# Optimization experiments

Measured on AMD Instinct MI355X. Metric: run time of the kernel, lower is better.

Reference implementation:

```python
import jax, jax.numpy as jnp
import numpy as np

N = 50000   # nodes
E = 200000  # edges (avg degree ~4, pose-graph-like sparsity)
F_IN = 512
NEG_SLOPE = 0.01  # F.leaky_relu default


def _softmax_aggr(src_feat, dst, num_nodes):
    # torch_geometric SoftmaxAggregation(t=1): per-destination, per-feature
    # alpha = softmax(x_j), out = sum_j alpha * x_j
    m = jax.ops.segment_max(src_feat, dst, num_segments=num_nodes)  # [N,F]
    m = jnp.where(jnp.isfinite(m), m, 0.0)  # empty segments -> -inf guard
    e = jnp.exp(src_feat - m[dst])                                   # [E,F]
    denom = jax.ops.segment_sum(e, dst, num_segments=num_nodes)      # [N,F]
    num = jax.ops.segment_sum(e * src_feat, dst, num_segments=num_nodes)
    return num / jnp.maximum(denom, 1e-16)  # 0 for isolated nodes


def setup_inputs() -> dict:
    key = jax.random.key(0)
    ks = jax.random.split(key, 9)
    inp = {
        "x": jax.random.normal(ks[0], (N, F_IN), dtype=jnp.float32),
        "W1_rel": jax.random.normal(ks[1], (513, 256), dtype=jnp.float32) * 0.04,
        "b1_rel": jnp.zeros((256,), dtype=jnp.float32),
        "W1_root": jax.random.normal(ks[2], (513, 256), dtype=jnp.float32) * 0.04,
        "W2_rel": jax.random.normal(ks[3], (257, 64), dtype=jnp.float32) * 0.06,
        "b2_rel": jnp.zeros((64,), dtype=jnp.float32),
        "W2_root": jax.random.normal(ks[4], (257, 64), dtype=jnp.float32) * 0.06,
        "Wp": jax.random.normal(ks[5], (65, 3), dtype=jnp.float32) * 0.1,
        "bp": jnp.zeros((3,), dtype=jnp.float32),
        "Wr": jax.random.normal(ks[6], (65, 4), dtype=jnp.float32) * 0.1,
        "br": jnp.zeros((4,), dtype=jnp.float32),
        "edge_index": jax.random.randint(ks[7], (2, E), 0, N, dtype=jnp.int64),
    }
    return inp


def reference(x, W1_rel, b1_rel, W1_root, W2_rel, b2_rel, W2_root,
              Wp, bp, Wr, br, edge_index):
    src, dst = edge_index[0], edge_index[1]
    node_index = jnp.arange(x.shape[0], dtype=x.dtype)[:, None]  # [N,1]

    # dropout is identity in eval mode
    h = jnp.concatenate([x, node_index], axis=1)  # [N,513]

    # GraphConv(513,256, aggr='softmax'): lin_rel(softmax_aggr(x_j)) + lin_root(x)
    agg1 = _softmax_aggr(h[src], dst, x.shape[0])               # [N,513]
    h = agg1 @ W1_rel + b1_rel + h @ W1_root                     # [N,256]
    h = jnp.where(h >= 0, h, NEG_SLOPE * h)

    h = jnp.concatenate([h, node_index], axis=1)  # [N,257]

    # GraphConv(257,64) default aggr='add'
    agg2 = jax.ops.segment_sum(h[src], dst, num_segments=x.shape[0])  # [N,257]
    h = agg2 @ W2_rel + b2_rel + h @ W2_root                           # [N,64]
    h = jnp.where(h >= 0, h, NEG_SLOPE * h)

    h = jnp.concatenate([h, node_index], axis=1)  # [N,65]

    position = h @ Wp + bp                         # [N,3]
    rotation = h @ Wr + br                         # [N,4]
    norm = jnp.linalg.norm(rotation, axis=1, keepdims=True)
    rotation = rotation / jnp.maximum(norm, 1e-12)  # F.normalize

    return jnp.concatenate([position, rotation], axis=1)  # [N,7]
```

## Files before the change

kernel.cpp:

```cpp
#include <hip/hip_runtime.h>

#define NNODES 50000
#define NEDGES 200000
#define NSCANB ((NNODES + 255) / 256)

typedef short  bf16x8 __attribute__((ext_vector_type(8)));
typedef float  f32x4  __attribute__((ext_vector_type(4)));
typedef unsigned int u32x4 __attribute__((ext_vector_type(4)));

__device__ __forceinline__ unsigned short f2bf(float f) {
    union { float f; unsigned int u; } c; c.f = f;
    unsigned int r = c.u + 0x7fffu + ((c.u >> 16) & 1u);
    return (unsigned short)(r >> 16);
}
__device__ __forceinline__ float bf2f(unsigned short h) {
    union { unsigned int u; float f; } c; c.u = ((unsigned int)h) << 16;
    return c.f;
}

#define PREP_Z NNODES
#define PREP_B1 (256 * 1024)
#define PREP_B2 (64 * 512)
#define PREP_XC (NNODES * 64)
#define PREP_TOT (PREP_Z + PREP_B1 + PREP_B2 + PREP_XC)
__global__ __launch_bounds__(256) void k_prep(const float* __restrict__ x,
                                              const float* __restrict__ W1_rel,
                                              const float* __restrict__ W1_root,
                                              const float* __restrict__ W2_rel,
                                              const float* __restrict__ W2_root,
                                              int* __restrict__ deg,
                                              unsigned short* __restrict__ Bt1,
                                              unsigned short* __restrict__ Bt2,
                                              unsigned short* __restrict__ xb) {
    int i = blockIdx.x * 256 + threadIdx.x;
    if (i < PREP_Z) { deg[i] = 0; return; }
    i -= PREP_Z;
    if (i < PREP_B1) {
        int n = i >> 10, k = i & 1023;
        float v = (k < 512) ? W1_rel[k * 256 + n] : W1_root[(k - 512) * 256 + n];
        Bt1[i] = f2bf(v);
        return;
    }
    i -= PREP_B1;
    if (i < PREP_B2) {
        int n = i >> 9, k = i & 511;
        float v = (k < 256) ? W2_rel[k * 64 + n] : W2_root[(k - 256) * 64 + n];
        Bt2[i] = f2bf(v);
        return;
    }
    i -= PREP_B2;
    if (i < PREP_XC) {
        int n = i >> 6, c8 = (i & 63) * 8;
        const float* xp = x + (size_t)n * 512 + c8;
        float4 a = *(const float4*)xp;
        float4 b = *(const float4*)(xp + 4);
        unsigned short o[8];
        o[0] = f2bf(a.x); o[1] = f2bf(a.y); o[2] = f2bf(a.z); o[3] = f2bf(a.w);
        o[4] = f2bf(b.x); o[5] = f2bf(b.y); o[6] = f2bf(b.z); o[7] = f2bf(b.w);
        *(u32x4*)(xb + (size_t)n * 512 + c8) = *(const u32x4*)o;
    }
}

__global__ void k_count(const int* __restrict__ ei, int* __restrict__ deg) {
    int e = blockIdx.x * 256 + threadIdx.x;
    if (e < NEDGES) atomicAdd(&deg[ei[NEDGES + e]], 1);
}

__global__ __launch_bounds__(256) void k_scanA(const int* __restrict__ deg,
                                               int* __restrict__ rs,
                                               int* __restrict__ partials) {
    __shared__ int sm[256];
    int t = threadIdx.x, i = blockIdx.x * 256 + t;
    int v = (i < NNODES) ? deg[i] : 0;
    sm[t] = v;
    __syncthreads();
#pragma unroll
    for (int off = 1; off < 256; off <<= 1) {
        int u = (t >= off) ? sm[t - off] : 0;
        __syncthreads();
        sm[t] += u;
        __syncthreads();
    }
    if (i < NNODES) rs[i] = sm[t] - v;
    if (t == 255) partials[blockIdx.x] = sm[255];
}

__global__ __launch_bounds__(256) void k_scanB(int* __restrict__ partials) {
    __shared__ int sm[256];
    int t = threadIdx.x;
    int v = (t < NSCANB) ? partials[t] : 0;
    sm[t] = v;
    __syncthreads();
#pragma unroll
    for (int off = 1; off < 256; off <<= 1) {
        int u = (t >= off) ? sm[t - off] : 0;
        __syncthreads();
        sm[t] += u;
        __syncthreads();
    }
    if (t < NSCANB) partials[t] = sm[t] - v;
}

__global__ __launch_bounds__(256) void k_scanC(int* __restrict__ rs,
                                               const int* __restrict__ partials,
                                               int* __restrict__ cursor) {
    int t = threadIdx.x, b = blockIdx.x, i = b * 256 + t;
    if (i < NNODES) {
        int v = rs[i] + partials[b];
        rs[i] = v;
        cursor[i] = v;
    }
    if (i == 0) rs[NNODES] = NEDGES;
}

__global__ void k_scatter(const int* __restrict__ ei, int* __restrict__ cursor,
                          int* __restrict__ srcs) {
    int e = blockIdx.x * 256 + threadIdx.x;
    if (e < NEDGES) {
        int d = ei[NEDGES + e];
        int p = atomicAdd(&cursor[d], 1);
        srcs[p] = ei[e];
    }
}

__global__ __launch_bounds__(256) void k_agg1(const unsigned short* __restrict__ xb,
                                              const int* __restrict__ rs,
                                              const int* __restrict__ srcs,
                                              unsigned short* __restrict__ AggBuf,
                                              float* __restrict__ aggidx,
                                              float* __restrict__ sidx) {
    int n = blockIdx.x;
    int t = threadIdx.x;
    int e0 = rs[n], e1 = rs[n + 1];
    float d0 = 0.f, q0 = 0.f, d1 = 0.f, q1 = 0.f;
    float mI = -INFINITY, dI = 0.f, qI = 0.f, sI = 0.f;
    for (int e = e0; e < e1; ++e) {
        int s = srcs[e];
        unsigned int v = *(const unsigned int*)(xb + (size_t)s * 512 + t * 2);
        float v0 = bf2f((unsigned short)(v & 0xffffu));
        float v1 = bf2f((unsigned short)(v >> 16));
        float e0v = __expf(v0);
        float e1v = __expf(v1);
        d0 += e0v; q0 += e0v * v0;
        d1 += e1v; q1 += e1v * v1;
        if (t == 0) {
            float vi = (float)s;
            sI += vi;
            float nm = fmaxf(mI, vi);
            float sc = __expf(mI - nm), ee = __expf(vi - nm);
            dI = dI * sc + ee;
            qI = qI * sc + ee * vi;
            mI = nm;
        }
    }
    float a0 = q0 / fmaxf(d0, 1e-16f);
    float a1 = q1 / fmaxf(d1, 1e-16f);
    unsigned int o = (unsigned int)f2bf(a0) | ((unsigned int)f2bf(a1) << 16);
    *(unsigned int*)(AggBuf + (size_t)n * 512 + t * 2) = o;
    if (t == 0) {
        aggidx[n] = qI / fmaxf(dI, 1e-16f);
        sidx[n] = sI;
    }
}

__global__ __launch_bounds__(256) void k_agg2(const int* __restrict__ rs,
                                              const int* __restrict__ srcs,
                                              const unsigned short* __restrict__ H1,
                                              unsigned short* __restrict__ Seg) {
    int half = threadIdx.x >> 7;
    int t = threadIdx.x & 127;
    int n = blockIdx.x * 2 + half;
    int e0 = rs[n], e1 = rs[n + 1];
    float a0 = 0.f, a1 = 0.f;
    for (int e = e0; e < e1; ++e) {
        int s = srcs[e];
        unsigned int v = *(const unsigned int*)(H1 + (size_t)s * 256 + t * 2);
        a0 += bf2f((unsigned short)(v & 0xffffu));
        a1 += bf2f((unsigned short)(v >> 16));
    }
    unsigned int o = (unsigned int)f2bf(a0) | ((unsigned int)f2bf(a1) << 16);
    *(unsigned int*)(Seg + (size_t)n * 256 + t * 2) = o;
}

__global__ __launch_bounds__(256, 5) void k_gemm1(const unsigned short* __restrict__ A1,
                                                  const unsigned short* __restrict__ A2,
                                                  const unsigned short* __restrict__ Bt,
                                                  const float* __restrict__ s1,
                                                  const float* __restrict__ r1,
                                                  const float* __restrict__ r2,
                                                  const float* __restrict__ bias,
                                                  unsigned short* __restrict__ outp) {
    constexpr int BM = 64, BN = 128, BK = 64;
    __shared__ __align__(16) unsigned short As[BM * BK];
    __shared__ __align__(16) unsigned short Bs[BN * BK];

    const int tid = threadIdx.x;
    const int w = tid >> 6;
    const int lane = tid & 63;
    const int lm = lane & 15;
    const int quad = lane >> 4;
    const int wr = w >> 1;
    const int wc = w & 1;
    const int rowbase = blockIdx.y * BM;
    const int colbase = blockIdx.x * BN;
    const int wrow = wr * 32;
    const int wcol = wc * 64;

    const int rsub = lane >> 3;
    const int csw = (lane & 7) ^ rsub;

    f32x4 acc[2][4];
#pragma unroll
    for (int mi = 0; mi < 2; ++mi)
#pragma unroll
        for (int ni = 0; ni < 4; ++ni) acc[mi][ni] = (f32x4){0.f, 0.f, 0.f, 0.f};

    for (int kt = 0; kt < 1024; kt += BK) {
        const unsigned short* Ab = (kt < 512) ? A1 : A2;
        int kof = (kt < 512) ? kt : kt - 512;
#pragma unroll
        for (int l = 0; l < 2; ++l) {
            int r = w * 16 + l * 8;
            int gr = rowbase + r + rsub;
            if (gr >= NNODES) gr = NNODES - 1;
            const unsigned short* gp = Ab + (size_t)gr * 512 + kof + csw * 8;
            __builtin_amdgcn_global_load_lds(
                (const __attribute__((address_space(1))) void*)gp,
                (__attribute__((address_space(3))) void*)(As + r * BK), 16, 0, 0);
        }
#pragma unroll
        for (int l = 0; l < 4; ++l) {
            int r = w * 32 + l * 8;
            const unsigned short* gp = Bt + (size_t)(colbase + r + rsub) * 1024 + kt + csw * 8;
            __builtin_amdgcn_global_load_lds(
                (const __attribute__((address_space(1))) void*)gp,
                (__attribute__((address_space(3))) void*)(Bs + r * BK), 16, 0, 0);
        }
        __syncthreads();
#pragma unroll
        for (int kk = 0; kk < BK; kk += 32) {
            const int kidx = (kk >> 3) + quad;
            const int phys = kidx ^ (lm & 7);
            bf16x8 af[2], bfr[4];
#pragma unroll
            for (int mi = 0; mi < 2; ++mi)
                af[mi] = __builtin_bit_cast(bf16x8,
                    *(const u32x4*)(As + (wrow + mi * 16 + lm) * BK + phys * 8));
#pragma unroll
            for (int ni = 0; ni < 4; ++ni)
                bfr[ni] = __builtin_bit_cast(bf16x8,
                    *(const u32x4*)(Bs + (wcol + ni * 16 + lm) * BK + phys * 8));
#pragma unroll
            for (int mi = 0; mi < 2; ++mi)
#pragma unroll
                for (int ni = 0; ni < 4; ++ni)
                    acc[mi][ni] = __builtin_amdgcn_mfma_f32_16x16x32_bf16(
                        af[mi], bfr[ni], acc[mi][ni], 0, 0, 0);
        }
        __syncthreads();
    }

#pragma unroll
    for (int ni = 0; ni < 4; ++ni) {
        int gc = colbase + wcol + ni * 16 + lm;
        float r1v = r1[gc], r2v = r2[gc], bv = bias[gc];
#pragma unroll
        for (int mi = 0; mi < 2; ++mi) {
#pragma unroll
            for (int r = 0; r < 4; ++r) {
                int grow = rowbase + wrow + mi * 16 + quad * 4 + r;
                if (grow < NNODES) {
                    float v = acc[mi][ni][r] + s1[grow] * r1v + (float)grow * r2v + bv;
                    v = (v >= 0.f) ? v : 0.01f * v;
                    outp[(size_t)grow * 256 + gc] = f2bf(v);
                }
            }
        }
    }
}

__global__ __launch_bounds__(256) void k_gemm2h(const unsigned short* __restrict__ A1,
                                                const unsigned short* __restrict__ A2,
                                                const unsigned short* __restrict__ Bt,
                                                const float* __restrict__ s1,
                                                const float* __restrict__ r1,
                                                const float* __restrict__ r2,
                                                const float* __restrict__ bias,
                                                const float* __restrict__ Wp,
                                                const float* __restrict__ bp,
                                                const float* __restrict__ Wr,
                                                const float* __restrict__ br,
                                                float* __restrict__ out) {
    constexpr int BM = 64, BN = 64, BK = 64;
    __shared__ __align__(16) unsigned short As[BM * BK];
    __shared__ __align__(16) unsigned short Bs[BN * BK];
    __shared__ float h2t[BM * 65];

    const int tid = threadIdx.x;
    const int w = tid >> 6;
    const int lane = tid & 63;
    const int lm = lane & 15;
    const int quad = lane >> 4;
    const int rowbase = blockIdx.x * BM;
    const int wrow = w * 16;

    const int rsub = lane >> 3;
    const int csw = (lane & 7) ^ rsub;

    f32x4 acc[4];
#pragma unroll
    for (int ni = 0; ni < 4; ++ni) acc[ni] = (f32x4){0.f, 0.f, 0.f, 0.f};

    for (int kt = 0; kt < 512; kt += BK) {
        const unsigned short* Ab = (kt < 256) ? A1 : A2;
        int kof = (kt < 256) ? kt : kt - 256;
#pragma unroll
        for (int l = 0; l < 2; ++l) {
            int r = w * 16 + l * 8;
            int gr = rowbase + r + rsub;
            if (gr >= NNODES) gr = NNODES - 1;
            const unsigned short* gp = Ab + (size_t)gr * 256 + kof + csw * 8;
            __builtin_amdgcn_global_load_lds(
                (const __attribute__((address_space(1))) void*)gp,
                (__attribute__((address_space(3))) void*)(As + r * BK), 16, 0, 0);
        }
#pragma unroll
        for (int l = 0; l < 2; ++l) {
            int r = w * 16 + l * 8;
            const unsigned short* gp = Bt + (size_t)(r + rsub) * 512 + kt + csw * 8;
            __builtin_amdgcn_global_load_lds(
                (const __attribute__((address_space(1))) void*)gp,
                (__attribute__((address_space(3))) void*)(Bs + r * BK), 16, 0, 0);
        }
        __syncthreads();
#pragma unroll
        for (int kk = 0; kk < BK; kk += 32) {
            const int kidx = (kk >> 3) + quad;
            const int phys = kidx ^ (lm & 7);
            bf16x8 af;
            af = __builtin_bit_cast(bf16x8,
                *(const u32x4*)(As + (wrow + lm) * BK + phys * 8));
            bf16x8 bfr[4];
#pragma unroll
            for (int ni = 0; ni < 4; ++ni)
                bfr[ni] = __builtin_bit_cast(bf16x8,
                    *(const u32x4*)(Bs + (ni * 16 + lm) * BK + phys * 8));
#pragma unroll
            for (int ni = 0; ni < 4; ++ni)
                acc[ni] = __builtin_amdgcn_mfma_f32_16x16x32_bf16(
                    af, bfr[ni], acc[ni], 0, 0, 0);
        }
        __syncthreads();
    }

#pragma unroll
    for (int ni = 0; ni < 4; ++ni) {
        int gc = ni * 16 + lm;
        float r1v = r1[gc], r2v = r2[gc], bv = bias[gc];
#pragma unroll
        for (int r = 0; r < 4; ++r) {
            int lrow = wrow + quad * 4 + r;
            int grow = rowbase + lrow;
            float v = acc[ni][r] + s1[grow < NNODES ? grow : 0] * r1v +
                      (float)grow * r2v + bv;
            v = (v >= 0.f) ? v : 0.01f * v;
            h2t[lrow * 65 + gc] = v;
        }
    }
    __syncthreads();

    if (tid < BM) {
        int grow = rowbase + tid;
        if (grow < NNODES) {
            const float* hv = h2t + tid * 65;
            float idx = (float)grow;
            float p0 = 0.f, p1 = 0.f, p2 = 0.f;
            float r0 = 0.f, r1a = 0.f, r2a = 0.f, r3 = 0.f;
#pragma unroll 8
            for (int c = 0; c < 64; ++c) {
                float v = hv[c];
                p0 += v * Wp[c * 3 + 0];
                p1 += v * Wp[c * 3 + 1];
                p2 += v * Wp[c * 3 + 2];
                r0 += v * Wr[c * 4 + 0];
                r1a += v * Wr[c * 4 + 1];
                r2a += v * Wr[c * 4 + 2];
                r3 += v * Wr[c * 4 + 3];
            }
            p0 += idx * Wp[64 * 3 + 0] + bp[0];
            p1 += idx * Wp[64 * 3 + 1] + bp[1];
            p2 += idx * Wp[64 * 3 + 2] + bp[2];
            r0 += idx * Wr[64 * 4 + 0] + br[0];
            r1a += idx * Wr[64 * 4 + 1] + br[1];
            r2a += idx * Wr[64 * 4 + 2] + br[2];
            r3 += idx * Wr[64 * 4 + 3] + br[3];
            float nrm = fmaxf(sqrtf(r0 * r0 + r1a * r1a + r2a * r2a + r3 * r3), 1e-12f);
            float* op = out + (size_t)grow * 7;
            op[0] = p0; op[1] = p1; op[2] = p2;
            op[3] = r0 / nrm; op[4] = r1a / nrm; op[5] = r2a / nrm; op[6] = r3 / nrm;
        }
    }
}

extern "C" void kernel_launch(void* const* d_in, const int* in_sizes, int n_in,
                              void* d_out, int out_size, void* d_ws, size_t ws_size,
                              hipStream_t stream) {
    const float* x       = (const float*)d_in[0];
    const float* W1_rel  = (const float*)d_in[1];
    const float* b1      = (const float*)d_in[2];
    const float* W1_root = (const float*)d_in[3];
    const float* W2_rel  = (const float*)d_in[4];
    const float* b2      = (const float*)d_in[5];
    const float* W2_root = (const float*)d_in[6];
    const float* Wp      = (const float*)d_in[7];
    const float* bp      = (const float*)d_in[8];
    const float* Wr      = (const float*)d_in[9];
    const float* br      = (const float*)d_in[10];
    const int*   ei      = (const int*)d_in[11];
    float* out = (float*)d_out;

    char* ws = (char*)d_ws;
    size_t off = 0;
    auto alloc = [&](size_t bytes) {
        size_t o = off;
        off = (off + bytes + 255) & ~(size_t)255;
        return (void*)(ws + o);
    };
    int*   deg       = (int*)alloc(NNODES * 4);
    int*   cursor    = (int*)alloc(NNODES * 4);
    int*   row_start = (int*)alloc((NNODES + 1) * 4);
    int*   srcs      = (int*)alloc(NEDGES * 4);
    int*   partials  = (int*)alloc(NSCANB * 4);
    float* aggidx    = (float*)alloc(NNODES * 4);
    float* sidx      = (float*)alloc(NNODES * 4);
    unsigned short* xb     = (unsigned short*)alloc((size_t)NNODES * 512 * 2);
    unsigned short* AggBuf = (unsigned short*)alloc((size_t)NNODES * 512 * 2);
    unsigned short* H1     = (unsigned short*)alloc((size_t)NNODES * 256 * 2);
    unsigned short* Seg    = (unsigned short*)alloc((size_t)NNODES * 256 * 2);
    unsigned short* Bt1    = (unsigned short*)alloc(256 * 1024 * 2);
    unsigned short* Bt2    = (unsigned short*)alloc(64 * 512 * 2);

    const int EB = (NEDGES + 255) / 256;

    k_prep<<<(PREP_TOT + 255) / 256, 256, 0, stream>>>(
        x, W1_rel, W1_root, W2_rel, W2_root, deg, Bt1, Bt2, xb);

    k_count<<<EB, 256, 0, stream>>>(ei, deg);
    k_scanA<<<NSCANB, 256, 0, stream>>>(deg, row_start, partials);
    k_scanB<<<1, 256, 0, stream>>>(partials);
    k_scanC<<<NSCANB, 256, 0, stream>>>(row_start, partials, cursor);
    k_scatter<<<EB, 256, 0, stream>>>(ei, cursor, srcs);

    k_agg1<<<NNODES, 256, 0, stream>>>(xb, row_start, srcs, AggBuf, aggidx, sidx);

    k_gemm1<<<dim3(2, (NNODES + 63) / 64), 256, 0, stream>>>(
        AggBuf, xb, Bt1, aggidx, W1_rel + 512 * 256, W1_root + 512 * 256, b1, H1);

    k_agg2<<<NNODES / 2, 256, 0, stream>>>(row_start, srcs, H1, Seg);

    k_gemm2h<<<(NNODES + 63) / 64, 256, 0, stream>>>(
        Seg, H1, Bt2, sidx, W2_rel + 256 * 64, W2_root + 256 * 64, b2,
        Wp, bp, Wr, br, out);
}
```

Measured before the change: 390.5 us.

## Precompute per-node exp weights in prep and move index aggregates into GEMM epilogues

The prep kernel now also computes exp(x) and x*exp(x) per feature as bf16 pairs into a new UW buffer, so the softmax aggregation only sums the precomputed numerator and denominator instead of evaluating exp per edge. The serial thread-0 node-index softmax and sum loops are removed from k_agg1 and recomputed inside the gemm1 and gemm2 epilogues from the CSR arrays. This removes exp work and the thread-0 serial tail from each agg1 block. In exchange, agg1 gathers 8 bytes per feature pair instead of 4, prep writes an extra 100MB buffer, and the exps are taken without max subtraction at bf16 precision.

```diff
diff --git a/kernel.cpp b/kernel.cpp
--- a/kernel.cpp
+++ b/kernel.cpp
@@ -15,6 +15,14 @@
 }
 __device__ __forceinline__ float bf2f(unsigned short h) {
     union { unsigned int u; float f; } c; c.u = ((unsigned int)h) << 16;
+    return c.f;
+}
+__device__ __forceinline__ float bflo(unsigned int v) {
+    union { unsigned int u; float f; } c; c.u = v << 16;
+    return c.f;
+}
+__device__ __forceinline__ float bfhi(unsigned int v) {
+    union { unsigned int u; float f; } c; c.u = v & 0xffff0000u;
     return c.f;
 }
 
@@ -31,7 +39,8 @@
                                               int* __restrict__ deg,
                                               unsigned short* __restrict__ Bt1,
                                               unsigned short* __restrict__ Bt2,
-                                              unsigned short* __restrict__ xb) {
+                                              unsigned short* __restrict__ xb,
+                                              uint2* __restrict__ UW) {
     int i = blockIdx.x * 256 + threadIdx.x;
     if (i < PREP_Z) { deg[i] = 0; return; }
     i -= PREP_Z;
@@ -54,10 +63,22 @@
         const float* xp = x + (size_t)n * 512 + c8;
         float4 a = *(const float4*)xp;
         float4 b = *(const float4*)(xp + 4);
+        float v[8] = {a.x, a.y, a.z, a.w, b.x, b.y, b.z, b.w};
         unsigned short o[8];
-        o[0] = f2bf(a.x); o[1] = f2bf(a.y); o[2] = f2bf(a.z); o[3] = f2bf(a.w);
-        o[4] = f2bf(b.x); o[5] = f2bf(b.y); o[6] = f2bf(b.z); o[7] = f2bf(b.w);
+        uint2 uw[4];
+#pragma unroll
+        for (int j = 0; j < 8; ++j) o[j] = f2bf(v[j]);
+#pragma unroll
+        for (int p = 0; p < 4; ++p) {
+            float v0 = v[2 * p], v1 = v[2 * p + 1];
+            float e0 = __expf(v0), e1 = __expf(v1);
+            uw[p].x = (unsigned int)f2bf(v0 * e0) | ((unsigned int)f2bf(v1 * e1) << 16);
+            uw[p].y = (unsigned int)f2bf(e0) | ((unsigned int)f2bf(e1) << 16);
+        }
         *(u32x4*)(xb + (size_t)n * 512 + c8) = *(const u32x4*)o;
+        uint2* uwp = UW + (size_t)n * 256 + (c8 >> 1);
+        *(u32x4*)uwp = *(const u32x4*)&uw[0];
+        *(u32x4*)(uwp + 2) = *(const u32x4*)&uw[2];
     }
 }
 
@@ -123,44 +144,24 @@
     }
 }
 
-__global__ __launch_bounds__(256) void k_agg1(const unsigned short* __restrict__ xb,
+__global__ __launch_bounds__(256) void k_agg1(const uint2* __restrict__ UW,
                                               const int* __restrict__ rs,
                                               const int* __restrict__ srcs,
-                                              unsigned short* __restrict__ AggBuf,
-                                              float* __restrict__ aggidx,
-                                              float* __restrict__ sidx) {
+                                              unsigned short* __restrict__ AggBuf) {
     int n = blockIdx.x;
     int t = threadIdx.x;
     int e0 = rs[n], e1 = rs[n + 1];
-    float d0 = 0.f, q0 = 0.f, d1 = 0.f, q1 = 0.f;
-    float mI = -INFINITY, dI = 0.f, qI = 0.f, sI = 0.f;
+    float nu0 = 0.f, nu1 = 0.f, de0 = 0.f, de1 = 0.f;
     for (int e = e0; e < e1; ++e) {
         int s = srcs[e];
-        unsigned int v = *(const unsigned int*)(xb + (size_t)s * 512 + t * 2);
-        float v0 = bf2f((unsigned short)(v & 0xffffu));
-        float v1 = bf2f((unsigned short)(v >> 16));
-        float e0v = __expf(v0);
-        float e1v = __expf(v1);
-        d0 += e0v; q0 += e0v * v0;
-        d1 += e1v; q1 += e1v * v1;
-        if (t == 0) {
-            float vi = (float)s;
-            sI += vi;
-            float nm = fmaxf(mI, vi);
-            float sc = __expf(mI - nm), ee = __expf(vi - nm);
-            dI = dI * sc + ee;
-            qI = qI * sc + ee * vi;
-            mI = nm;
-        }
-    }
-    float a0 = q0 / fmaxf(d0, 1e-16f);
-    float a1 = q1 / fmaxf(d1, 1e-16f);
+        uint2 vw = UW[(size_t)s * 256 + t];
+        nu0 += bflo(vw.x); nu1 += bfhi(vw.x);
+        de0 += bflo(vw.y); de1 += bfhi(vw.y);
+    }
+    float a0 = nu0 / fmaxf(de0, 1e-16f);
+    float a1 = nu1 / fmaxf(de1, 1e-16f);
     unsigned int o = (unsigned int)f2bf(a0) | ((unsigned int)f2bf(a1) << 16);
     *(unsigned int*)(AggBuf + (size_t)n * 512 + t * 2) = o;
-    if (t == 0) {
-        aggidx[n] = qI / fmaxf(dI, 1e-16f);
-        sidx[n] = sI;
-    }
 }
 
 __global__ __launch_bounds__(256) void k_agg2(const int* __restrict__ rs,
@@ -185,7 +186,8 @@
 __global__ __launch_bounds__(256, 5) void k_gemm1(const unsigned short* __restrict__ A1,
                                                   const unsigned short* __restrict__ A2,
                                                   const unsigned short* __restrict__ Bt,
-                                                  const float* __restrict__ s1,
+                                                  const int* __restrict__ rs,
+                                                  const int* __restrict__ srcs,
                                                   const float* __restrict__ r1,
                                                   const float* __restrict__ r2,
                                                   const float* __restrict__ bias,
@@ -193,6 +195,7 @@
     constexpr int BM = 64, BN = 128, BK = 64;
     __shared__ __align__(16) unsigned short As[BM * BK];
     __shared__ __align__(16) unsigned short Bs[BN * BK];
+    __shared__ float s1t[BM];
 
     const int tid = threadIdx.x;
     const int w = tid >> 6;
@@ -260,6 +263,26 @@
         __syncthreads();
     }
 
+    if (tid < BM) {
+        int grow = rowbase + tid;
+        float r_ = 0.f;
+        if (grow < NNODES) {
+            int e0 = rs[grow], e1 = rs[grow + 1];
+            float m = -INFINITY, d = 0.f, q = 0.f;
+            for (int e = e0; e < e1; ++e) {
+                float v = (float)srcs[e];
+                float nm = fmaxf(m, v);
+                float sc = __expf(m - nm), ee = __expf(v - nm);
+                d = d * sc + ee;
+                q = q * sc + ee * v;
+                m = nm;
+            }
+            r_ = q / fmaxf(d, 1e-16f);
+        }
+        s1t[tid] = r_;
+    }
+    __syncthreads();
+
 #pragma unroll
     for (int ni = 0; ni < 4; ++ni) {
         int gc = colbase + wcol + ni * 16 + lm;
@@ -268,9 +291,10 @@
         for (int mi = 0; mi < 2; ++mi) {
 #pragma unroll
             for (int r = 0; r < 4; ++r) {
-                int grow = rowbase + wrow + mi * 16 + quad * 4 + r;
+                int lrow = wrow + mi * 16 + quad * 4 + r;
+                int grow = rowbase + lrow;
                 if (grow < NNODES) {
-                    float v = acc[mi][ni][r] + s1[grow] * r1v + (float)grow * r2v + bv;
+                    float v = acc[mi][ni][r] + s1t[lrow] * r1v + (float)grow * r2v + bv;
                     v = (v >= 0.f) ? v : 0.01f * v;
                     outp[(size_t)grow * 256 + gc] = f2bf(v);
                 }
@@ -282,7 +306,8 @@
 __global__ __launch_bounds__(256) void k_gemm2h(const unsigned short* __restrict__ A1,
                                                 const unsigned short* __restrict__ A2,
                                                 const unsigned short* __restrict__ Bt,
-                                                const float* __restrict__ s1,
+                                                const int* __restrict__ rs,
+                                                const int* __restrict__ srcs,
                                                 const float* __restrict__ r1,
                                                 const float* __restrict__ r2,
                                                 const float* __restrict__ bias,
@@ -295,6 +320,7 @@
     __shared__ __align__(16) unsigned short As[BM * BK];
     __shared__ __align__(16) unsigned short Bs[BN * BK];
     __shared__ float h2t[BM * 65];
+    __shared__ float s1t[BM];
 
     const int tid = threadIdx.x;
     const int w = tid >> 6;
@@ -353,6 +379,17 @@
         __syncthreads();
     }
 
+    if (tid < BM) {
+        int grow = rowbase + tid;
+        float si = 0.f;
+        if (grow < NNODES) {
+            int e0 = rs[grow], e1 = rs[grow + 1];
+            for (int e = e0; e < e1; ++e) si += (float)srcs[e];
+        }
+        s1t[tid] = si;
+    }
+    __syncthreads();
+
 #pragma unroll
     for (int ni = 0; ni < 4; ++ni) {
         int gc = ni * 16 + lm;
@@ -361,8 +398,7 @@
         for (int r = 0; r < 4; ++r) {
             int lrow = wrow + quad * 4 + r;
             int grow = rowbase + lrow;
-            float v = acc[ni][r] + s1[grow < NNODES ? grow : 0] * r1v +
-                      (float)grow * r2v + bv;
+            float v = acc[ni][r] + s1t[lrow] * r1v + (float)grow * r2v + bv;
             v = (v >= 0.f) ? v : 0.01f * v;
             h2t[lrow * 65 + gc] = v;
         }
@@ -431,9 +467,8 @@
     int*   row_start = (int*)alloc((NNODES + 1) * 4);
     int*   srcs      = (int*)alloc(NEDGES * 4);
     int*   partials  = (int*)alloc(NSCANB * 4);
-    float* aggidx    = (float*)alloc(NNODES * 4);
-    float* sidx      = (float*)alloc(NNODES * 4);
     unsigned short* xb     = (unsigned short*)alloc((size_t)NNODES * 512 * 2);
+    uint2* UW              = (uint2*)alloc((size_t)NNODES * 256 * 8);
     unsigned short* AggBuf = (unsigned short*)alloc((size_t)NNODES * 512 * 2);
     unsigned short* H1     = (unsigned short*)alloc((size_t)NNODES * 256 * 2);
     unsigned short* Seg    = (unsigned short*)alloc((size_t)NNODES * 256 * 2);
@@ -443,7 +478,7 @@
     const int EB = (NEDGES + 255) / 256;
 
     k_prep<<<(PREP_TOT + 255) / 256, 256, 0, stream>>>(
-        x, W1_rel, W1_root, W2_rel, W2_root, deg, Bt1, Bt2, xb);
+        x, W1_rel, W1_root, W2_rel, W2_root, deg, Bt1, Bt2, xb, UW);
 
     k_count<<<EB, 256, 0, stream>>>(ei, deg);
     k_scanA<<<NSCANB, 256, 0, stream>>>(deg, row_start, partials);
@@ -451,14 +486,14 @@
     k_scanC<<<NSCANB, 256, 0, stream>>>(row_start, partials, cursor);
     k_scatter<<<EB, 256, 0, stream>>>(ei, cursor, srcs);
 
-    k_agg1<<<NNODES, 256, 0, stream>>>(xb, row_start, srcs, AggBuf, aggidx, sidx);
+    k_agg1<<<NNODES, 256, 0, stream>>>(UW, row_start, srcs, AggBuf);
 
     k_gemm1<<<dim3(2, (NNODES + 63) / 64), 256, 0, stream>>>(
-        AggBuf, xb, Bt1, aggidx, W1_rel + 512 * 256, W1_root + 512 * 256, b1, H1);
+        AggBuf, xb, Bt1, row_start, srcs, W1_rel + 512 * 256, W1_root + 512 * 256, b1, H1);
 
     k_agg2<<<NNODES / 2, 256, 0, stream>>>(row_start, srcs, H1, Seg);
 
     k_gemm2h<<<(NNODES + 63) / 64, 256, 0, stream>>>(
-        Seg, H1, Bt2, sidx, W2_rel + 256 * 64, W2_root + 256 * 64, b2,
+        Seg, H1, Bt2, row_start, srcs, W2_rel + 256 * 64, W2_root + 256 * 64, b2,
         Wp, bp, Wr, br, out);
 }
```

Result: slower. 418.6 us (+7.2%).
